# Performance work log

Hardware: AMD Instinct MI355X
Metric: run time of the kernel (lower is better)

## Reference

```python
import jax, jax.numpy as jnp
import numpy as np

EMBED_DIM = 1024
NUM_HEADS = 16
HEAD_DIM = EMBED_DIM // NUM_HEADS


def setup_inputs() -> dict:
    key = jax.random.key(0)
    ks = jax.random.split(key, 6)
    B, S, D = 4, 2048, EMBED_DIM
    std = 1.0 / np.sqrt(D)
    x = jax.random.normal(ks[0], (B, S, D), dtype=jnp.float32)
    wq = jax.random.normal(ks[1], (D, D), dtype=jnp.float32) * std
    wk = jax.random.normal(ks[2], (D, D), dtype=jnp.float32) * std
    wv = jax.random.normal(ks[3], (D, D), dtype=jnp.float32) * std
    wo = jax.random.normal(ks[4], (D, D), dtype=jnp.float32) * std
    bo = jax.random.normal(ks[5], (D,), dtype=jnp.float32) * 0.01
    return {"x": x, "wq": wq, "wk": wk, "wv": wv, "wo": wo, "bo": bo}


def reference(x, wq, wk, wv, wo, bo):
    B, S, D = x.shape
    H, Hd = NUM_HEADS, HEAD_DIM
    scale = 1.0 / jnp.sqrt(jnp.asarray(Hd, x.dtype))
    # nn.Linear computes x @ W.T; split into heads -> [B, H, S, Hd]
    q = (x @ wq.T).reshape(B, S, H, Hd).transpose(0, 2, 1, 3)
    k = (x @ wk.T).reshape(B, S, H, Hd).transpose(0, 2, 1, 3)
    v = (x @ wv.T).reshape(B, S, H, Hd).transpose(0, 2, 1, 3)
    scores = jnp.einsum("bhqd,bhkd->bhqk", q, k) * scale  # [B,H,S,S]
    attn = jax.nn.softmax(scores, axis=-1)
    ctx = jnp.einsum("bhqk,bhkd->bhqd", attn, v)
    ctx = ctx.transpose(0, 2, 1, 3).reshape(B, S, D)
    return ctx @ wo.T + bo
```

## Files before the change

### kernel.cpp

```cpp
#include <hip/hip_runtime.h>

typedef __bf16 bf16x8 __attribute__((ext_vector_type(8)));
typedef __bf16 bf16x4 __attribute__((ext_vector_type(4)));
typedef float f32x4 __attribute__((ext_vector_type(4)));
typedef unsigned u32x4 __attribute__((ext_vector_type(4)));
typedef unsigned short u16;

#define GAS __attribute__((address_space(1)))
#define LAS __attribute__((address_space(3)))

static __device__ __forceinline__ void gload16(const void* g, void* l) {
  __builtin_amdgcn_global_load_lds((const GAS unsigned int*)g, (LAS unsigned int*)l, 16, 0, 0);
}

static __device__ __forceinline__ u16 f2bf(float f) {
  unsigned u = __builtin_bit_cast(unsigned, f);
  u += 0x7fffu + ((u >> 16) & 1u);
  return (u16)(u >> 16);
}

static __device__ __forceinline__ unsigned pk2(float lo, float hi) {
  ushort2 u;
  u.x = __builtin_bit_cast(u16, (__bf16)lo);
  u.y = __builtin_bit_cast(u16, (__bf16)hi);
  return __builtin_bit_cast(unsigned, u);
}

static __device__ __forceinline__ f32x4 vmax4(f32x4 a, f32x4 b) {
  f32x4 r;
  r[0] = fmaxf(a[0], b[0]); r[1] = fmaxf(a[1], b[1]);
  r[2] = fmaxf(a[2], b[2]); r[3] = fmaxf(a[3], b[3]);
  return r;
}

__global__ void cvt_kernel(const float* __restrict__ src, u16* __restrict__ dst, int n4) {
  int i = blockIdx.x * 256 + threadIdx.x;
  if (i >= n4) return;
  float4 v = reinterpret_cast<const float4*>(src)[i];
  ushort4 o;
  o.x = f2bf(v.x); o.y = f2bf(v.y); o.z = f2bf(v.z); o.w = f2bf(v.w);
  reinterpret_cast<ushort4*>(dst)[i] = o;
}

__global__ void cvt_w_kernel(const float* __restrict__ w0, const float* __restrict__ w1,
                             const float* __restrict__ w2, const float* __restrict__ w3,
                             u16* __restrict__ d0, u16* __restrict__ d1,
                             u16* __restrict__ d2, u16* __restrict__ d3) {
  int sel = blockIdx.x >> 10;
  int i = (blockIdx.x & 1023) * 256 + threadIdx.x;
  const float* s = sel == 0 ? w0 : sel == 1 ? w1 : sel == 2 ? w2 : w3;
  u16* d = sel == 0 ? d0 : sel == 1 ? d1 : sel == 2 ? d2 : d3;
  float4 v = reinterpret_cast<const float4*>(s)[i];
  ushort4 o;
  o.x = f2bf(v.x); o.y = f2bf(v.y); o.z = f2bf(v.z); o.w = f2bf(v.w);
  reinterpret_cast<ushort4*>(d)[i] = o;
}

__global__ void gemm_qkv(const u16* __restrict__ A, const u16* __restrict__ W,
                         u16* __restrict__ Qo, u16* __restrict__ Ko, u16* __restrict__ Vo) {
  __shared__ u16 As[128 * 32];
  __shared__ u16 Bs[128 * 32];
  const int t = threadIdx.x;
  const int lane = t & 63;
  const int w = t >> 6;
  const int wr = w >> 1, wc = w & 1;
  const int l15 = lane & 15, lhi = lane >> 4;
  const int swz = (blockIdx.x & 7) * 192 + (blockIdx.x >> 3);
  const int bm = swz / 24, bn = swz % 24;

  f32x4 acc[4][4];
#pragma unroll
  for (int a = 0; a < 4; ++a)
#pragma unroll
    for (int b = 0; b < 4; ++b) acc[a][b] = (f32x4){0.f, 0.f, 0.f, 0.f};

  const u16* ag = A + (size_t)(bm * 128 + (t >> 2)) * 1024 + (t & 3) * 8;
  const u16* bg = W + (size_t)(bn * 128 + (t >> 2)) * 1024 + (t & 3) * 8;
  u16* as_p = &As[t * 8];
  u16* bs_p = &Bs[t * 8];

  for (int kt = 0; kt < 32; ++kt) {
    gload16(ag, as_p);
    gload16(ag + 64 * 1024, as_p + 2048);
    gload16(bg, bs_p);
    gload16(bg + 64 * 1024, bs_p + 2048);
    ag += 32; bg += 32;
    __syncthreads();
    bf16x8 af[4], bfr[4];
#pragma unroll
    for (int mt = 0; mt < 4; ++mt)
      af[mt] = *(const bf16x8*)&As[(wr * 64 + mt * 16 + l15) * 32 + lhi * 8];
#pragma unroll
    for (int nt = 0; nt < 4; ++nt)
      bfr[nt] = *(const bf16x8*)&Bs[(wc * 64 + nt * 16 + l15) * 32 + lhi * 8];
#pragma unroll
    for (int mt = 0; mt < 4; ++mt)
#pragma unroll
      for (int nt = 0; nt < 4; ++nt)
        acc[mt][nt] = __builtin_amdgcn_mfma_f32_16x16x32_bf16(af[mt], bfr[nt], acc[mt][nt], 0, 0, 0);
    __syncthreads();
  }

  const int tsel = bn >> 3;
  const int m0 = bm * 128 + wr * 64;
  const int n0 = bn * 128 + wc * 64;
  const int bb = bm >> 4;
  if (tsel == 0) {
    const float qs = 0.125f * 1.4426950408889634f;
#pragma unroll
    for (int nt = 0; nt < 4; ++nt) {
      int n = n0 + nt * 16 + l15;
      int c = n & 1023, h = c >> 6, hd = c & 63;
      size_t base = (size_t)(bb * 16 + h) * 2048 * 64 + hd;
#pragma unroll
      for (int mt = 0; mt < 4; ++mt)
#pragma unroll
        for (int i = 0; i < 4; ++i) {
          int s = (m0 + mt * 16 + lhi * 4 + i) & 2047;
          Qo[base + (size_t)s * 64] = f2bf(acc[mt][nt][i] * qs);
        }
    }
  } else if (tsel == 1) {
#pragma unroll
    for (int nt = 0; nt < 4; ++nt) {
      int n = n0 + nt * 16 + l15;
      int c = n & 1023, h = c >> 6, hd = c & 63;
      size_t base = (size_t)(bb * 16 + h) * 2048 * 64 + hd;
#pragma unroll
      for (int mt = 0; mt < 4; ++mt)
#pragma unroll
        for (int i = 0; i < 4; ++i) {
          int s = (m0 + mt * 16 + lhi * 4 + i) & 2047;
          Ko[base + (size_t)s * 64] = f2bf(acc[mt][nt][i]);
        }
    }
  } else {
#pragma unroll
    for (int nt = 0; nt < 4; ++nt) {
      int n = n0 + nt * 16 + l15;
      int c = n & 1023, h = c >> 6, hd = c & 63;
#pragma unroll
      for (int mt = 0; mt < 4; ++mt) {
        int s0 = (m0 + mt * 16 + lhi * 4) & 2047;
        ushort4 pk;
        pk.x = f2bf(acc[mt][nt][0]);
        pk.y = f2bf(acc[mt][nt][1]);
        pk.z = f2bf(acc[mt][nt][2]);
        pk.w = f2bf(acc[mt][nt][3]);
        *(ushort4*)&Vo[((size_t)(bb * 16 + h) * 64 + hd) * 2048 + s0] = pk;
      }
    }
  }
}

__global__ __launch_bounds__(256, 2) void attn_kernel(const u16* __restrict__ Q,
                                                      const u16* __restrict__ K,
                                                      const u16* __restrict__ Vt,
                                                      u16* __restrict__ Ctx) {
  __shared__ u16 Ks[2][128 * 64];
  __shared__ u16 Vs[2][64 * 128];
  const int t = threadIdx.x;
  const int lane = t & 63;
  const int w = t >> 6;
  const int l15 = lane & 15, lhi = lane >> 4;
  const int swz = (blockIdx.x & 7) * 128 + (blockIdx.x >> 3);
  const int qt = swz & 15, pair = swz >> 4;
  const u16* qp = Q + (size_t)pair * 2048 * 64;
  const u16* kp = K + (size_t)pair * 2048 * 64;
  const u16* vp = Vt + (size_t)pair * 64 * 2048;

  const int qrA = qt * 128 + w * 32 + l15;
  bf16x8 qfA[2], qfB[2];
  qfA[0] = *(const bf16x8*)&qp[(size_t)qrA * 64 + lhi * 8];
  qfA[1] = *(const bf16x8*)&qp[(size_t)qrA * 64 + 32 + lhi * 8];
  qfB[0] = *(const bf16x8*)&qp[(size_t)(qrA + 16) * 64 + lhi * 8];
  qfB[1] = *(const bf16x8*)&qp[(size_t)(qrA + 16) * 64 + 32 + lhi * 8];

  float mA = -1e30f, lA = 0.f, mB = -1e30f, lB = 0.f;
  f32x4 coA[4], coB[4];
#pragma unroll
  for (int n = 0; n < 4; ++n) { coA[n] = (f32x4){0.f, 0.f, 0.f, 0.f}; coB[n] = coA[n]; }

  auto stage = [&](int b, int tt) {
#pragma unroll
    for (int j = 0; j < 4; ++j) {
      int r = j * 32 + (t >> 3);
      int c0 = (t & 7) * 8;
      gload16(kp + (size_t)(tt * 128 + r) * 64 + (c0 ^ ((r & 7) << 3)), &Ks[b][j * 2048 + t * 8]);
    }
#pragma unroll
    for (int j = 0; j < 4; ++j) {
      int r = j * 16 + (t >> 4);
      int c0 = (t & 15) * 8;
      gload16(vp + (size_t)r * 2048 + tt * 128 + (c0 ^ ((r & 7) << 3)), &Vs[b][j * 2048 + t * 8]);
    }
  };

  auto softmax_step = [&](f32x4 (&sa)[8], float& m, float& l, f32x4 (&co)[4],
                          unsigned (&pw)[8][2]) {
    f32x4 t0 = vmax4(sa[0], sa[1]);
    f32x4 t1 = vmax4(sa[2], sa[3]);
    f32x4 t2 = vmax4(sa[4], sa[5]);
    f32x4 t3 = vmax4(sa[6], sa[7]);
    t0 = vmax4(t0, t1);
    t2 = vmax4(t2, t3);
    t0 = vmax4(t0, t2);
    float mx = fmaxf(fmaxf(t0[0], t0[1]), fmaxf(t0[2], t0[3]));
    mx = fmaxf(mx, __shfl_xor(mx, 16));
    mx = fmaxf(mx, __shfl_xor(mx, 32));
    float mn = m;
    if (!__all(mx - m <= 8.0f)) {
      mn = fmaxf(m, mx);
      float sc = __builtin_exp2f(m - mn);
      l *= sc;
      float si0 = __shfl(sc, lhi * 4 + 0);
      float si1 = __shfl(sc, lhi * 4 + 1);
      float si2 = __shfl(sc, lhi * 4 + 2);
      float si3 = __shfl(sc, lhi * 4 + 3);
#pragma unroll
      for (int nthd = 0; nthd < 4; ++nthd) {
        co[nthd][0] *= si0; co[nthd][1] *= si1;
        co[nthd][2] *= si2; co[nthd][3] *= si3;
      }
      m = mn;
    }
#pragma unroll
    for (int nt = 0; nt < 8; ++nt)
#pragma unroll
      for (int e = 0; e < 4; ++e) sa[nt][e] = __builtin_exp2f(sa[nt][e] - mn);
    f32x4 s0 = sa[0] + sa[1];
    f32x4 s1 = sa[2] + sa[3];
    f32x4 s2 = sa[4] + sa[5];
    f32x4 s3 = sa[6] + sa[7];
    s0 = s0 + s1; s2 = s2 + s3; s0 = s0 + s2;
    float rs = (s0[0] + s0[1]) + (s0[2] + s0[3]);
    rs += __shfl_xor(rs, 16);
    rs += __shfl_xor(rs, 32);
    l += rs;
#pragma unroll
    for (int nt = 0; nt < 8; ++nt) {
      pw[nt][0] = pk2(sa[nt][0], sa[nt][1]);
      pw[nt][1] = pk2(sa[nt][2], sa[nt][3]);
    }
  };

  stage(0, 0);
  __syncthreads();

  for (int kt = 0; kt < 16; ++kt) {
    const int cur = kt & 1;
    if (kt < 15) stage(cur ^ 1, kt + 1);

    f32x4 saA[8], saB[8];
#pragma unroll
    for (int nt = 0; nt < 8; ++nt) {
      saA[nt] = (f32x4){0.f, 0.f, 0.f, 0.f};
      saB[nt] = saA[nt];
#pragma unroll
      for (int ks = 0; ks < 2; ++ks) {
        int r = nt * 16 + l15;
        int c = (ks * 32 + lhi * 8) ^ ((r & 7) << 3);
        bf16x8 kf = *(const bf16x8*)&Ks[cur][r * 64 + c];
        saA[nt] = __builtin_amdgcn_mfma_f32_16x16x32_bf16(kf, qfA[ks], saA[nt], 0, 0, 0);
        saB[nt] = __builtin_amdgcn_mfma_f32_16x16x32_bf16(kf, qfB[ks], saB[nt], 0, 0, 0);
      }
    }

    unsigned pwA[8][2], pwB[8][2];
    softmax_step(saA, mA, lA, coA, pwA);
    softmax_step(saB, mB, lB, coB, pwB);

#pragma unroll
    for (int ks = 0; ks < 4; ++ks) {
      u32x4 awA = {pwA[2 * ks][0], pwA[2 * ks][1], pwA[2 * ks + 1][0], pwA[2 * ks + 1][1]};
      u32x4 awB = {pwB[2 * ks][0], pwB[2 * ks][1], pwB[2 * ks + 1][0], pwB[2 * ks + 1][1]};
      bf16x8 afA = __builtin_bit_cast(bf16x8, awA);
      bf16x8 afB = __builtin_bit_cast(bf16x8, awB);
#pragma unroll
      for (int nthd = 0; nthd < 4; ++nthd) {
        int row = nthd * 16 + l15;
        int swzr = (row & 7) << 3;
        int c0 = (ks * 32 + lhi * 4) ^ swzr;
        int c1 = (ks * 32 + 16 + lhi * 4) ^ swzr;
        bf16x4 v0 = *(const bf16x4*)&Vs[cur][row * 128 + c0];
        bf16x4 v1 = *(const bf16x4*)&Vs[cur][row * 128 + c1];
        bf16x8 vf;
#pragma unroll
        for (int e = 0; e < 4; ++e) { vf[e] = v0[e]; vf[e + 4] = v1[e]; }
        coA[nthd] = __builtin_amdgcn_mfma_f32_16x16x32_bf16(afA, vf, coA[nthd], 0, 0, 0);
        coB[nthd] = __builtin_amdgcn_mfma_f32_16x16x32_bf16(afB, vf, coB[nthd], 0, 0, 0);
      }
    }
    __syncthreads();
  }

  float liA[4], liB[4];
#pragma unroll
  for (int i = 0; i < 4; ++i) {
    liA[i] = 1.0f / __shfl(lA, lhi * 4 + i);
    liB[i] = 1.0f / __shfl(lB, lhi * 4 + i);
  }
  const int bb = pair >> 4, h = pair & 15;
  const int sbase = qt * 128 + w * 32 + lhi * 4;
#pragma unroll
  for (int nthd = 0; nthd < 4; ++nthd) {
    int hd = nthd * 16 + l15;
#pragma unroll
    for (int i = 0; i < 4; ++i) {
      Ctx[(size_t)(bb * 2048 + sbase + i) * 1024 + h * 64 + hd] = f2bf(coA[nthd][i] * liA[i]);
      Ctx[(size_t)(bb * 2048 + sbase + 16 + i) * 1024 + h * 64 + hd] = f2bf(coB[nthd][i] * liB[i]);
    }
  }
}

__global__ void gemm_out(const u16* __restrict__ A, const u16* __restrict__ W,
                         const float* __restrict__ Bo, float* __restrict__ Out) {
  __shared__ u16 As[128 * 32];
  __shared__ u16 Bs[128 * 32];
  const int t = threadIdx.x;
  const int lane = t & 63;
  const int w = t >> 6;
  const int wr = w >> 1, wc = w & 1;
  const int l15 = lane & 15, lhi = lane >> 4;
  const int swz = (blockIdx.x & 7) * 64 + (blockIdx.x >> 3);
  const int bm = swz >> 3, bn = swz & 7;

  f32x4 acc[4][4];
#pragma unroll
  for (int a = 0; a < 4; ++a)
#pragma unroll
    for (int b = 0; b < 4; ++b) acc[a][b] = (f32x4){0.f, 0.f, 0.f, 0.f};

  const u16* ag = A + (size_t)(bm * 128 + (t >> 2)) * 1024 + (t & 3) * 8;
  const u16* bg = W + (size_t)(bn * 128 + (t >> 2)) * 1024 + (t & 3) * 8;
  u16* as_p = &As[t * 8];
  u16* bs_p = &Bs[t * 8];

  for (int kt = 0; kt < 32; ++kt) {
    gload16(ag, as_p);
    gload16(ag + 64 * 1024, as_p + 2048);
    gload16(bg, bs_p);
    gload16(bg + 64 * 1024, bs_p + 2048);
    ag += 32; bg += 32;
    __syncthreads();
    bf16x8 af[4], bfr[4];
#pragma unroll
    for (int mt = 0; mt < 4; ++mt)
      af[mt] = *(const bf16x8*)&As[(wr * 64 + mt * 16 + l15) * 32 + lhi * 8];
#pragma unroll
    for (int nt = 0; nt < 4; ++nt)
      bfr[nt] = *(const bf16x8*)&Bs[(wc * 64 + nt * 16 + l15) * 32 + lhi * 8];
#pragma unroll
    for (int mt = 0; mt < 4; ++mt)
#pragma unroll
      for (int nt = 0; nt < 4; ++nt)
        acc[mt][nt] = __builtin_amdgcn_mfma_f32_16x16x32_bf16(af[mt], bfr[nt], acc[mt][nt], 0, 0, 0);
    __syncthreads();
  }

  const int m0 = bm * 128 + wr * 64;
  const int n0 = bn * 128 + wc * 64;
#pragma unroll
  for (int nt = 0; nt < 4; ++nt) {
    int n = n0 + nt * 16 + l15;
    float bias = Bo[n];
#pragma unroll
    for (int mt = 0; mt < 4; ++mt)
#pragma unroll
      for (int i = 0; i < 4; ++i) {
        int m = m0 + mt * 16 + lhi * 4 + i;
        Out[(size_t)m * 1024 + n] = acc[mt][nt][i] + bias;
      }
  }
}

extern "C" void kernel_launch(void* const* d_in, const int* in_sizes, int n_in,
                              void* d_out, int out_size, void* d_ws, size_t ws_size,
                              hipStream_t stream) {
  const float* x  = (const float*)d_in[0];
  const float* wq = (const float*)d_in[1];
  const float* wk = (const float*)d_in[2];
  const float* wv = (const float*)d_in[3];
  const float* wo = (const float*)d_in[4];
  const float* bo = (const float*)d_in[5];
  float* out = (float*)d_out;

  u16* xb    = (u16*)d_ws;
  u16* wqkvb = xb + (size_t)8 * 1024 * 1024;
  u16* wob   = wqkvb + (size_t)3 * 1024 * 1024;
  u16* qb    = wob + (size_t)1 * 1024 * 1024;
  u16* kb    = qb + (size_t)8 * 1024 * 1024;
  u16* vtb   = kb + (size_t)8 * 1024 * 1024;
  u16* ctxb  = xb;

  cvt_kernel<<<8192, 256, 0, stream>>>(x, xb, 2097152);
  cvt_w_kernel<<<4096, 256, 0, stream>>>(wq, wk, wv, wo,
                                         wqkvb, wqkvb + 1048576, wqkvb + 2097152, wob);
  gemm_qkv<<<64 * 24, 256, 0, stream>>>(xb, wqkvb, qb, kb, vtb);
  attn_kernel<<<1024, 256, 0, stream>>>(qb, kb, vtb, ctxb);
  gemm_out<<<64 * 8, 256, 0, stream>>>(ctxb, wob, bo, out);
}
```

Baseline: 249.6 us.

## Enlarge attention tiles to 256 queries, permute V layout, add MFMA priority hints

The attention kernel now runs 512-thread blocks covering 256 query rows per head, so each K/V tile staged in LDS serves twice as many queries and per-query staging traffic is halved. The QKV GEMM writes V^T with a permuted sequence order, which lets the PV stage read each MFMA operand with one 16-byte LDS load instead of two 8-byte loads plus a shuffle. s_setprio raises wave priority around the MFMA sections, and LDS offsets are hoisted out of the loop. Costs: launch bounds of 512 threads with 4 waves per SIMD cap register use, and there are half as many blocks to spread across the CUs.

```diff
diff --git a/kernel.cpp b/kernel.cpp
--- a/kernel.cpp
+++ b/kernel.cpp
@@ -1,7 +1,6 @@
 #include <hip/hip_runtime.h>
 
 typedef __bf16 bf16x8 __attribute__((ext_vector_type(8)));
-typedef __bf16 bf16x4 __attribute__((ext_vector_type(4)));
 typedef float f32x4 __attribute__((ext_vector_type(4)));
 typedef unsigned u32x4 __attribute__((ext_vector_type(4)));
 typedef unsigned short u16;
@@ -142,68 +141,71 @@
 #pragma unroll
       for (int mt = 0; mt < 4; ++mt) {
         int s0 = (m0 + mt * 16 + lhi * 4) & 2047;
+        int sp0 = ((s0 >> 4) & 1) * 4 + ((s0 >> 2) & 3) * 8 + (s0 >> 5) * 32;
         ushort4 pk;
         pk.x = f2bf(acc[mt][nt][0]);
         pk.y = f2bf(acc[mt][nt][1]);
         pk.z = f2bf(acc[mt][nt][2]);
         pk.w = f2bf(acc[mt][nt][3]);
-        *(ushort4*)&Vo[((size_t)(bb * 16 + h) * 64 + hd) * 2048 + s0] = pk;
+        *(ushort4*)&Vo[((size_t)(bb * 16 + h) * 64 + hd) * 2048 + sp0] = pk;
       }
     }
   }
 }
 
-__global__ __launch_bounds__(256, 2) void attn_kernel(const u16* __restrict__ Q,
+__global__ __launch_bounds__(512, 4) void attn_kernel(const u16* __restrict__ Q,
                                                       const u16* __restrict__ K,
-                                                      const u16* __restrict__ Vt,
+                                                      const u16* __restrict__ Vp,
                                                       u16* __restrict__ Ctx) {
-  __shared__ u16 Ks[2][128 * 64];
-  __shared__ u16 Vs[2][64 * 128];
+  __shared__ u16 Ks[2 * 128 * 64];
+  __shared__ u16 Vs[2 * 64 * 128];
   const int t = threadIdx.x;
   const int lane = t & 63;
   const int w = t >> 6;
   const int l15 = lane & 15, lhi = lane >> 4;
-  const int swz = (blockIdx.x & 7) * 128 + (blockIdx.x >> 3);
-  const int qt = swz & 15, pair = swz >> 4;
+  const int swz = (blockIdx.x & 7) * 64 + (blockIdx.x >> 3);
+  const int pair = swz >> 3, qt = swz & 7;
   const u16* qp = Q + (size_t)pair * 2048 * 64;
   const u16* kp = K + (size_t)pair * 2048 * 64;
-  const u16* vp = Vt + (size_t)pair * 64 * 2048;
-
-  const int qrA = qt * 128 + w * 32 + l15;
+  const u16* vp = Vp + (size_t)pair * 64 * 2048;
+
+  const int qrA = qt * 256 + w * 32 + l15;
   bf16x8 qfA[2], qfB[2];
   qfA[0] = *(const bf16x8*)&qp[(size_t)qrA * 64 + lhi * 8];
   qfA[1] = *(const bf16x8*)&qp[(size_t)qrA * 64 + 32 + lhi * 8];
   qfB[0] = *(const bf16x8*)&qp[(size_t)(qrA + 16) * 64 + lhi * 8];
   qfB[1] = *(const bf16x8*)&qp[(size_t)(qrA + 16) * 64 + 32 + lhi * 8];
 
+  const int swzq = (l15 & 7) << 3;
+  const int kofs0 = l15 * 64 + ((lhi * 8) ^ swzq);
+  const int kofs1 = l15 * 64 + ((32 + lhi * 8) ^ swzq);
+  const int vofs0 = l15 * 128 + ((lhi * 8) ^ swzq);
+  const int vofs1 = l15 * 128 + ((32 + lhi * 8) ^ swzq);
+
   float mA = -1e30f, lA = 0.f, mB = -1e30f, lB = 0.f;
   f32x4 coA[4], coB[4];
 #pragma unroll
   for (int n = 0; n < 4; ++n) { coA[n] = (f32x4){0.f, 0.f, 0.f, 0.f}; coB[n] = coA[n]; }
 
-  auto stage = [&](int b, int tt) {
-#pragma unroll
-    for (int j = 0; j < 4; ++j) {
-      int r = j * 32 + (t >> 3);
-      int c0 = (t & 7) * 8;
-      gload16(kp + (size_t)(tt * 128 + r) * 64 + (c0 ^ ((r & 7) << 3)), &Ks[b][j * 2048 + t * 8]);
-    }
-#pragma unroll
-    for (int j = 0; j < 4; ++j) {
-      int r = j * 16 + (t >> 4);
-      int c0 = (t & 15) * 8;
-      gload16(vp + (size_t)r * 2048 + tt * 128 + (c0 ^ ((r & 7) << 3)), &Vs[b][j * 2048 + t * 8]);
+  auto stage = [&](int cb, int tt) {
+#pragma unroll
+    for (int j = 0; j < 2; ++j) {
+      int c = j * 512 + t;
+      int r = c >> 3, c8 = (c & 7) * 8;
+      gload16(kp + (size_t)(tt * 128 + r) * 64 + (c8 ^ ((r & 7) << 3)), &Ks[cb + c * 8]);
+    }
+#pragma unroll
+    for (int j = 0; j < 2; ++j) {
+      int c = j * 512 + t;
+      int r = c >> 4, c8 = (c & 15) * 8;
+      gload16(vp + (size_t)r * 2048 + tt * 128 + (c8 ^ ((r & 7) << 3)), &Vs[cb + c * 8]);
     }
   };
 
   auto softmax_step = [&](f32x4 (&sa)[8], float& m, float& l, f32x4 (&co)[4],
                           unsigned (&pw)[8][2]) {
-    f32x4 t0 = vmax4(sa[0], sa[1]);
-    f32x4 t1 = vmax4(sa[2], sa[3]);
-    f32x4 t2 = vmax4(sa[4], sa[5]);
-    f32x4 t3 = vmax4(sa[6], sa[7]);
-    t0 = vmax4(t0, t1);
-    t2 = vmax4(t2, t3);
+    f32x4 t0 = vmax4(vmax4(sa[0], sa[1]), vmax4(sa[2], sa[3]));
+    f32x4 t2 = vmax4(vmax4(sa[4], sa[5]), vmax4(sa[6], sa[7]));
     t0 = vmax4(t0, t2);
     float mx = fmaxf(fmaxf(t0[0], t0[1]), fmaxf(t0[2], t0[3]));
     mx = fmaxf(mx, __shfl_xor(mx, 16));
@@ -228,11 +230,9 @@
     for (int nt = 0; nt < 8; ++nt)
 #pragma unroll
       for (int e = 0; e < 4; ++e) sa[nt][e] = __builtin_exp2f(sa[nt][e] - mn);
-    f32x4 s0 = sa[0] + sa[1];
-    f32x4 s1 = sa[2] + sa[3];
-    f32x4 s2 = sa[4] + sa[5];
-    f32x4 s3 = sa[6] + sa[7];
-    s0 = s0 + s1; s2 = s2 + s3; s0 = s0 + s2;
+    f32x4 s0 = (sa[0] + sa[1]) + (sa[2] + sa[3]);
+    f32x4 s2 = (sa[4] + sa[5]) + (sa[6] + sa[7]);
+    s0 = s0 + s2;
     float rs = (s0[0] + s0[1]) + (s0[2] + s0[3]);
     rs += __shfl_xor(rs, 16);
     rs += __shfl_xor(rs, 32);
@@ -248,49 +248,45 @@
   __syncthreads();
 
   for (int kt = 0; kt < 16; ++kt) {
-    const int cur = kt & 1;
-    if (kt < 15) stage(cur ^ 1, kt + 1);
+    const int cb = (kt & 1) * 8192;
+    if (kt < 15) stage(cb ^ 8192, kt + 1);
 
     f32x4 saA[8], saB[8];
+    __builtin_amdgcn_s_setprio(1);
 #pragma unroll
     for (int nt = 0; nt < 8; ++nt) {
       saA[nt] = (f32x4){0.f, 0.f, 0.f, 0.f};
       saB[nt] = saA[nt];
-#pragma unroll
-      for (int ks = 0; ks < 2; ++ks) {
-        int r = nt * 16 + l15;
-        int c = (ks * 32 + lhi * 8) ^ ((r & 7) << 3);
-        bf16x8 kf = *(const bf16x8*)&Ks[cur][r * 64 + c];
-        saA[nt] = __builtin_amdgcn_mfma_f32_16x16x32_bf16(kf, qfA[ks], saA[nt], 0, 0, 0);
-        saB[nt] = __builtin_amdgcn_mfma_f32_16x16x32_bf16(kf, qfB[ks], saB[nt], 0, 0, 0);
-      }
-    }
+      bf16x8 kf0 = *(const bf16x8*)&Ks[cb + kofs0 + nt * 1024];
+      bf16x8 kf1 = *(const bf16x8*)&Ks[cb + kofs1 + nt * 1024];
+      saA[nt] = __builtin_amdgcn_mfma_f32_16x16x32_bf16(kf0, qfA[0], saA[nt], 0, 0, 0);
+      saB[nt] = __builtin_amdgcn_mfma_f32_16x16x32_bf16(kf0, qfB[0], saB[nt], 0, 0, 0);
+      saA[nt] = __builtin_amdgcn_mfma_f32_16x16x32_bf16(kf1, qfA[1], saA[nt], 0, 0, 0);
+      saB[nt] = __builtin_amdgcn_mfma_f32_16x16x32_bf16(kf1, qfB[1], saB[nt], 0, 0, 0);
+    }
+    __builtin_amdgcn_s_setprio(0);
 
     unsigned pwA[8][2], pwB[8][2];
     softmax_step(saA, mA, lA, coA, pwA);
     softmax_step(saB, mB, lB, coB, pwB);
 
+    __builtin_amdgcn_s_setprio(1);
 #pragma unroll
     for (int ks = 0; ks < 4; ++ks) {
       u32x4 awA = {pwA[2 * ks][0], pwA[2 * ks][1], pwA[2 * ks + 1][0], pwA[2 * ks + 1][1]};
       u32x4 awB = {pwB[2 * ks][0], pwB[2 * ks][1], pwB[2 * ks + 1][0], pwB[2 * ks + 1][1]};
       bf16x8 afA = __builtin_bit_cast(bf16x8, awA);
       bf16x8 afB = __builtin_bit_cast(bf16x8, awB);
+      const int vo = (ks & 1) ? vofs1 : vofs0;
+      const int vhi = (ks >> 1) * 64;
 #pragma unroll
       for (int nthd = 0; nthd < 4; ++nthd) {
-        int row = nthd * 16 + l15;
-        int swzr = (row & 7) << 3;
-        int c0 = (ks * 32 + lhi * 4) ^ swzr;
-        int c1 = (ks * 32 + 16 + lhi * 4) ^ swzr;
-        bf16x4 v0 = *(const bf16x4*)&Vs[cur][row * 128 + c0];
-        bf16x4 v1 = *(const bf16x4*)&Vs[cur][row * 128 + c1];
-        bf16x8 vf;
-#pragma unroll
-        for (int e = 0; e < 4; ++e) { vf[e] = v0[e]; vf[e + 4] = v1[e]; }
+        bf16x8 vf = *(const bf16x8*)&Vs[cb + vo + vhi + nthd * 2048];
         coA[nthd] = __builtin_amdgcn_mfma_f32_16x16x32_bf16(afA, vf, coA[nthd], 0, 0, 0);
         coB[nthd] = __builtin_amdgcn_mfma_f32_16x16x32_bf16(afB, vf, coB[nthd], 0, 0, 0);
       }
     }
+    __builtin_amdgcn_s_setprio(0);
     __syncthreads();
   }
 
@@ -301,7 +297,7 @@
     liB[i] = 1.0f / __shfl(lB, lhi * 4 + i);
   }
   const int bb = pair >> 4, h = pair & 15;
-  const int sbase = qt * 128 + w * 32 + lhi * 4;
+  const int sbase = qt * 256 + w * 32 + lhi * 4;
 #pragma unroll
   for (int nthd = 0; nthd < 4; ++nthd) {
     int hd = nthd * 16 + l15;
@@ -397,6 +393,6 @@
   cvt_w_kernel<<<4096, 256, 0, stream>>>(wq, wk, wv, wo,
                                          wqkvb, wqkvb + 1048576, wqkvb + 2097152, wob);
   gemm_qkv<<<64 * 24, 256, 0, stream>>>(xb, wqkvb, qb, kb, vtb);
-  attn_kernel<<<1024, 256, 0, stream>>>(qb, kb, vtb, ctxb);
+  attn_kernel<<<512, 512, 0, stream>>>(qb, kb, vtb, ctxb);
   gemm_out<<<64 * 8, 256, 0, stream>>>(ctxb, wob, bo, out);
 }
```

Result: slower. 261.1 us (+4.6%).
